# Performance work log

Measured on AMD Instinct MI355X. Metric: run time of the kernel, lower is better.

Reference implementation:

```python
import jax, jax.numpy as jnp
import numpy as np

NEG_SLOPE = 0.2  # PyG GATConv default negative_slope


def gat_conv(x, edge_index, W, att_src, att_dst, bias):
    # PyG GATConv, heads=1, add_self_loops=True, lin bias=False, final bias added
    N = x.shape[0]
    h = x @ W                                     # [N, F]
    loops = jnp.arange(N, dtype=edge_index.dtype)
    src = jnp.concatenate([edge_index[0], loops])
    dst = jnp.concatenate([edge_index[1], loops])
    a_src = h @ att_src                           # [N]
    a_dst = h @ att_dst                           # [N]
    e = a_src[src] + a_dst[dst]
    e = jnp.where(e > 0, e, NEG_SLOPE * e)        # leaky_relu
    m = jax.ops.segment_max(e, dst, num_segments=N)
    w = jnp.exp(e - m[dst])
    denom = jax.ops.segment_sum(w, dst, num_segments=N)
    alpha = w / denom[dst]
    out = jax.ops.segment_sum(h[src] * alpha[:, None], dst, num_segments=N)
    return out + bias


def gcn_conv(x, edge_index, W, b):
    # PyG GCNConv: add self-loops + symmetric normalization
    N = x.shape[0]
    loops = jnp.arange(N, dtype=edge_index.dtype)
    src = jnp.concatenate([edge_index[0], loops])
    dst = jnp.concatenate([edge_index[1], loops])
    deg = jax.ops.segment_sum(jnp.ones(src.shape[0], dtype=x.dtype), dst, num_segments=N)
    dinv = jax.lax.rsqrt(jnp.maximum(deg, 1e-12))  # deg >= 1 thanks to self-loops
    norm = dinv[src] * dinv[dst]
    xw = x @ W
    return jax.ops.segment_sum(xw[src] * norm[:, None], dst, num_segments=N) + b


def get_final_node(x, batch, num_graphs):
    nn_ = jax.ops.segment_sum(jnp.ones(x.shape[0], dtype=jnp.int32), batch, num_segments=num_graphs)
    cum = jnp.concatenate([jnp.zeros(1, dtype=nn_.dtype), jnp.cumsum(nn_)[:-1]])
    return x[cum]


def ontology_emb(table, e1, e2, W, asrc, adst, b, idx_map):
    emb = gat_conv(table, e1, W, asrc, adst, b)
    emb = gat_conv(emb, e2, W, asrc, adst, b)
    return emb[idx_map]


def _forward(spec_emb, diag_table, proce_table, atc_table,
             diag_W, diag_asrc, diag_adst, diag_b,
             proce_W, proce_asrc, proce_adst, proce_b,
             atc_W, atc_asrc, atc_adst, atc_b,
             gcn_W1, gcn_b1, gcn_W2, gcn_b2, gcn_W3, gcn_b3,
             diag_e1, diag_e2, proce_e1, proce_e2, atc_e1, atc_e2,
             diag_map, proce_map, atc_map,
             left_x, left_graph_index, right_x, right_graph_index,
             left_x_batch, right_x_batch, num_graphs):
    diag_emb = ontology_emb(diag_table, diag_e1, diag_e2, diag_W, diag_asrc, diag_adst, diag_b, diag_map)
    proce_emb = ontology_emb(proce_table, proce_e1, proce_e2, proce_W, proce_asrc, proce_adst, proce_b, proce_map)
    atc_emb = ontology_emb(atc_table, atc_e1, atc_e2, atc_W, atc_asrc, atc_adst, atc_b, atc_map)
    all_emb = jnp.concatenate([spec_emb, diag_emb, proce_emb, atc_emb], axis=0)
    lh = all_emb[left_x[:, 0]]   # squeeze(dim=1)
    rh = all_emb[right_x[:, 0]]
    for W, b in ((gcn_W1, gcn_b1), (gcn_W2, gcn_b2), (gcn_W3, gcn_b3)):
        lh = gcn_conv(lh, left_graph_index, W, b)
        rh = gcn_conv(rh, right_graph_index, W, b)
    lf = get_final_node(lh, left_x_batch, num_graphs)
    rf = get_final_node(rh, right_x_batch, num_graphs)
    eps = 1e-6  # CosineSimilarity eps
    num = jnp.sum(lf * rf, axis=-1)
    den = jnp.maximum(jnp.linalg.norm(lf, axis=-1), eps) * jnp.maximum(jnp.linalg.norm(rf, axis=-1), eps)
    return num / den


def setup_inputs() -> dict:
    key = jax.random.key(0)
    ks = jax.random.split(key, 32)
    HID = 128
    B, NPG = 2048, 50
    N = B * NPG               # 102400 nodes per side
    E_PAT = 409600            # 4 edges per node
    DIAG_N, DIAG_L = 30000, 20000
    PROCE_N, PROCE_L = 12000, 8000
    ATC_N, ATC_L = 6000, 4000
    ALL = 1 + DIAG_L + PROCE_L + ATC_L
    f = lambda k, s: jax.random.normal(k, s, dtype=jnp.float32)
    scale = 0.1
    inp = {
        'spec_emb': f(ks[0], (1, HID)),
        'diag_table': f(ks[1], (DIAG_N, HID)),
        'proce_table': f(ks[2], (PROCE_N, HID)),
        'atc_table': f(ks[3], (ATC_N, HID)),
    }
    for i, nm in enumerate(['diag', 'proce', 'atc']):
        inp[nm + '_W'] = f(ks[4 + i], (HID, HID)) * scale
        inp[nm + '_asrc'] = f(ks[7 + i], (HID,)) * scale
        inp[nm + '_adst'] = f(ks[10 + i], (HID,)) * scale
        inp[nm + '_b'] = jnp.zeros((HID,), jnp.float32)
    for j in range(3):
        inp['gcn_W%d' % (j + 1)] = f(ks[13 + j], (HID, HID)) * scale
        inp['gcn_b%d' % (j + 1)] = jnp.zeros((HID,), jnp.float32)
    inp['diag_e1'] = jax.random.randint(ks[16], (2, DIAG_N), 0, DIAG_N, dtype=jnp.int32)
    inp['diag_e2'] = jax.random.randint(ks[17], (2, DIAG_N), 0, DIAG_N, dtype=jnp.int32)
    inp['proce_e1'] = jax.random.randint(ks[18], (2, PROCE_N), 0, PROCE_N, dtype=jnp.int32)
    inp['proce_e2'] = jax.random.randint(ks[19], (2, PROCE_N), 0, PROCE_N, dtype=jnp.int32)
    inp['atc_e1'] = jax.random.randint(ks[20], (2, ATC_N), 0, ATC_N, dtype=jnp.int32)
    inp['atc_e2'] = jax.random.randint(ks[21], (2, ATC_N), 0, ATC_N, dtype=jnp.int32)
    inp['diag_map'] = jnp.arange(DIAG_L, dtype=jnp.int32)
    inp['proce_map'] = jnp.arange(PROCE_L, dtype=jnp.int32)
    inp['atc_map'] = jnp.arange(ATC_L, dtype=jnp.int32)
    inp['left_x'] = jax.random.randint(ks[22], (N, 1), 0, ALL, dtype=jnp.int32)
    inp['right_x'] = jax.random.randint(ks[23], (N, 1), 0, ALL, dtype=jnp.int32)
    inp['left_graph_index'] = jax.random.randint(ks[24], (2, E_PAT), 0, N, dtype=jnp.int32)
    inp['right_graph_index'] = jax.random.randint(ks[25], (2, E_PAT), 0, N, dtype=jnp.int32)
    batch = jnp.repeat(jnp.arange(B, dtype=jnp.int32), NPG)
    inp['left_x_batch'] = batch
    inp['right_x_batch'] = batch
    inp['num_graphs'] = B
    return inp


def reference(spec_emb, diag_table, proce_table, atc_table,
              diag_W, diag_asrc, diag_adst, diag_b,
              proce_W, proce_asrc, proce_adst, proce_b,
              atc_W, atc_asrc, atc_adst, atc_b,
              gcn_W1, gcn_b1, gcn_W2, gcn_b2, gcn_W3, gcn_b3,
              diag_e1, diag_e2, proce_e1, proce_e2, atc_e1, atc_e2,
              diag_map, proce_map, atc_map,
              left_x, left_graph_index, right_x, right_graph_index,
              left_x_batch, right_x_batch, num_graphs):
    return _forward(spec_emb, diag_table, proce_table, atc_table,
                    diag_W, diag_asrc, diag_adst, diag_b,
                    proce_W, proce_asrc, proce_adst, proce_b,
                    atc_W, atc_asrc, atc_adst, atc_b,
                    gcn_W1, gcn_b1, gcn_W2, gcn_b2, gcn_W3, gcn_b3,
                    diag_e1, diag_e2, proce_e1, proce_e2, atc_e1, atc_e2,
                    diag_map, proce_map, atc_map,
                    left_x, left_graph_index, right_x, right_graph_index,
                    left_x_batch, right_x_batch, num_graphs)
```

## Files before the change

kernel.cpp:

```cpp
#include <hip/hip_runtime.h>
#include <hip/hip_bf16.h>

#define HID 128

typedef unsigned int uint;
typedef unsigned short ushort;
typedef short short8 __attribute__((ext_vector_type(8)));
typedef float f32x4 __attribute__((ext_vector_type(4)));

static inline int cdiv_i(long a, long b) { return (int)((a + b - 1) / b); }
static inline int imax_i(int a, int b) { return a > b ? a : b; }

__device__ __forceinline__ float bf2f(uint hi) {
    return __builtin_bit_cast(float, hi << 16);
}
__device__ __forceinline__ ushort f2bf(float f) {
    uint u = __builtin_bit_cast(uint, f);
    u = (u + 0x7fffu + ((u >> 16) & 1u)) >> 16;
    return (ushort)u;
}

struct CsrDesc {
    const int* esrc[8];
    const int* edst[8];
    int ebase[9];
    int nbase[9];
    int totE;
};

template <typename AT>
__device__ __forceinline__ void load_afrag(const AT* __restrict__ A, long row,
                                           int koff, short8& af) {
    if constexpr (__is_same(AT, ushort)) {
        const uint4 raw = *(const uint4*)(A + row * 128 + koff);
        af = __builtin_bit_cast(short8, raw);
    } else {
        const float4* p = (const float4*)(A + row * 128 + koff);
        const float4 x0 = p[0], x1 = p[1];
        af[0] = (short)f2bf(x0.x); af[1] = (short)f2bf(x0.y);
        af[2] = (short)f2bf(x0.z); af[3] = (short)f2bf(x0.w);
        af[4] = (short)f2bf(x1.x); af[5] = (short)f2bf(x1.y);
        af[6] = (short)f2bf(x1.z); af[7] = (short)f2bf(x1.w);
    }
}

struct GOnto {
    const ushort* Wt0; const ushort* Wt1; const ushort* Wt2;
    const float* s0; const float* s1; const float* s2;
    const float* d0; const float* d1; const float* d2;
    int bs1, bs2;
    int r1, r2, r3;
};
// ... 57 lines not shown
                if (row < Mg) Hg[row * 128 + col] = f2bf(acc[mi][ni][reg]);
            }
        }
    }

    float asv[8], adv[8];
#pragma unroll
    for (int ni = 0; ni < 8; ++ni) {
        asv[ni] = avs[ni * 16 + r];
        adv[ni] = avd[ni * 16 + r];
    }
#pragma unroll
    for (int mi = 0; mi < 2; ++mi) {
#pragma unroll
        for (int reg = 0; reg < 4; ++reg) {
            float ps = 0.f, pd = 0.f;
#pragma unroll
            for (int ni = 0; ni < 8; ++ni) {
                ps += acc[mi][ni][reg] * asv[ni];
                pd += acc[mi][ni][reg] * adv[ni];
            }
#pragma unroll
            for (int o = 1; o < 16; o <<= 1) {
                ps += __shfl_xor(ps, o);
                pd += __shfl_xor(pd, o);
            }
            const long row = m0 + mi * 16 + q * 4 + reg;
            if (r == 0 && row < Mg) {
                as_o[rb + row] = ps;
                ad_o[rb + row] = pd;
            }
        }
    }
}

__global__ __launch_bounds__(256) void gemm_onto_l2(const ushort* __restrict__ x0,
                                                    const ushort* __restrict__ x1,
                                                    const ushort* __restrict__ x2,
                                                    GOnto g, ushort* __restrict__ H,
                                                    float* __restrict__ as_o,
                                                    float* __restrict__ ad_o) {
    gemm_onto_dev<ushort>(blockIdx.x, x0, x1, x2, g, H, as_o, ad_o);
}

struct EmbSrc {
    const float* spec; const ushort* oE;
    const int* m0; const int* m1; const int* m2;
    int lb2, lb3, r1, r2;
};

__device__ __forceinline__ short8 load_emb(const EmbSrc& e, long row, int koff) {
    short8 af;
    if (row == 0) {
        const float4* pp = (const float4*)(e.spec + koff);
        const float4 x0 = pp[0], x1 = pp[1];
        af[0] = (short)f2bf(x0.x); af[1] = (short)f2bf(x0.y);
        af[2] = (short)f2bf(x0.z); af[3] = (short)f2bf(x0.w);
        af[4] = (short)f2bf(x1.x); af[5] = (short)f2bf(x1.y);
        af[6] = (short)f2bf(x1.z); af[7] = (short)f2bf(x1.w);
        return af;
    }
    const int r = (int)row;
    const int seg = (r >= e.lb2) + (r >= e.lb3);
    const int local = r - ((seg == 0) ? 1 : (seg == 1) ? e.lb2 : e.lb3);
    const int* mp = (seg == 0) ? e.m0 : (seg == 1) ? e.m1 : e.m2;
    const int rb = (seg == 0) ? 0 : (seg == 1) ? e.r1 : e.r2;
    const long sr = (long)rb + mp[local];
    return __builtin_bit_cast(short8, *(const uint4*)(e.oE + sr * 128 + koff));
}

__device__ void gemm_pat_tile(const EmbSrc& es, const ushort* __restrict__ Wt,
                              ushort* __restrict__ C, long m0blk, long rowEnd) {
    const int tid = threadIdx.x;
    const int wave = tid >> 6, lane = tid & 63;
    const int r = lane & 15, q = lane >> 4;
// ... 47 lines not shown
    gemm_pat_tile(es, Wt, C, m0, M);
    if (m0 + 128 < M) gemm_pat_tile(es, Wt, C, m0 + 128, M);
}

__device__ __forceinline__ void fold1_dev(int idx, const float* __restrict__ W2,
                                          const float* __restrict__ b2,
                                          const float* __restrict__ W3,
                                          float* __restrict__ W23b) {
    if (idx >= 129 * 128) return;
    const int i = idx >> 7, j = idx & 127;
    const float* a = (i < 128) ? (W2 + i * 128) : b2;
    float s = 0.f;
#pragma unroll 8
    for (int k = 0; k < 128; ++k) s += a[k] * W3[k * 128 + j];
    W23b[idx] = s;
}

__device__ __forceinline__ void fold2_dev(int idx, const float* __restrict__ W1,
                                          const float* __restrict__ b1,
                                          const float* __restrict__ W23b,
                                          ushort* __restrict__ WpT,
                                          float* __restrict__ cbuf) {
    if (idx >= 130 * 128) return;
    const int i = idx >> 7, j = idx & 127;
    if (i == 129) { cbuf[128 + j] = W23b[128 * 128 + j]; return; }
    const float* a = (i < 128) ? (W1 + i * 128) : b1;
    float s = 0.f;
#pragma unroll 8
    for (int k = 0; k < 128; ++k) s += a[k] * W23b[k * 128 + j];
    if (i < 128) WpT[j * 128 + i] = f2bf(s);
    else cbuf[j] = s;
}

__device__ __forceinline__ void mark_dev(int i, const int* __restrict__ lEg,
                                         const int* __restrict__ rEg, int EP,
                                         int NP, int* __restrict__ mk,
                                         int testBit, int setBit) {
    int src, dst;
    if (i < 2 * EP) {
        const int side = i >= EP;
        const int e = i - side * EP;
        const int* eg = side ? rEg : lEg;
        src = side * NP + eg[e];
        dst = side * NP + eg[EP + e];
    } else if (i < 2 * EP + 2 * NP) {
        src = dst = i - 2 * EP;
    } else return;
    if (mk[dst] & testBit) {
        const int old = mk[src];
        if (!(old & setBit)) mk[src] = old | setBit;
    }
}

__device__ __forceinline__ void csr_count_dev(int i, const CsrDesc& d,
                                              int* __restrict__ cnt) {
    if (i >= d.totE) return;
    int li = 0;
#pragma unroll
    for (int k = 1; k < 8; ++k) li += (i >= d.ebase[k]);
    const int v = d.nbase[li] + d.edst[li][i - d.ebase[li]];
    atomicAdd(&cnt[v], 1);
}

struct PackPrep {
    const float* W2; const float* b2; const float* W3; float* W23b;
    const float* wsrc[3]; ushort* wt_out;
    int* cnt; int NV;
    const int* bL; const int* bR; int NP;
    int* gfL; int* gfR; int* mk;
    int nbF1, nbWT, nbInit;
};

__global__ __launch_bounds__(256) void k_prep(PackPrep p) {
    const int b = blockIdx.x, tid = threadIdx.x;
    if (b < p.nbF1) {
        fold1_dev(b * 256 + tid, p.W2, p.b2, p.W3, p.W23b);
    } else if (b < p.nbF1 + p.nbWT) {
        const int idx = (b - p.nbF1) * 256 + tid;
        if (idx < 3 * 16384) {
            const int m = idx >> 14;
            const int e = idx & 16383;
            const int n = e >> 7, k = e & 127;
            p.wt_out[idx] = f2bf(p.wsrc[m][k * 128 + n]);
        }
    } else {
        const int i = (b - p.nbF1 - p.nbWT) * 256 + tid;
        if (i < p.NV) p.cnt[i] = 0;
        if (i < 2 * p.NP) {
            const int side = i >= p.NP;
            const int ii = i - (side ? p.NP : 0);
            const int* bb = side ? p.bR : p.bL;
            int* gf = side ? p.gfR : p.gfL;
            const int cur = bb[ii];
            const int prev = (ii == 0) ? -1 : bb[ii - 1];
            int m = 0;
            if (cur > prev) {
                for (int g = prev + 1; g <= cur; ++g) gf[g] = ii;
                m = 1;
            }
            p.mk[i] = m;
        }
    }
}

struct PackBig {
    const float* x0; const float* x1; const float* x2;
    GOnto go; ushort* H; float* as_o; float* ad_o;
    const float* W1; const float* b1; const float* W23b;
    ushort* WpT; float* cbuf;
    CsrDesc dsc; int* cnt;
    const int* lEg; const int* rEg; int EP; int NP; int* mk;
    int nbGemm, nbF2, nbCnt;
};

__global__ __launch_bounds__(256) void k_big1(PackBig p) {
    const int b = blockIdx.x, tid = threadIdx.x;
    if (b < p.nbGemm) {
        gemm_onto_dev<float>(b, p.x0, p.x1, p.x2, p.go, p.H, p.as_o, p.ad_o);
    } else if (b < p.nbGemm + p.nbF2) {
        fold2_dev((b - p.nbGemm) * 256 + tid, p.W1, p.b1, p.W23b, p.WpT, p.cbuf);
    } else if (b < p.nbGemm + p.nbF2 + p.nbCnt) {
        csr_count_dev((b - p.nbGemm - p.nbF2) * 256 + tid, p.dsc, p.cnt);
    } else {
        mark_dev((b - p.nbGemm - p.nbF2 - p.nbCnt) * 256 + tid, p.lEg, p.rEg,
                 p.EP, p.NP, p.mk, 1, 2);
    }
}

__device__ void scan_tile_dev(const int* __restrict__ in, int* __restrict__ out,
                              int* __restrict__ bsum, int n, int pn0, int pcnt,
                              float* __restrict__ dinv, int tb, int tid,
                              int* sbuf) {
    const int base = tb * 1024 + tid * 4;
    int v[4];
    int s = 0;
#pragma unroll
    for (int k = 0; k < 4; ++k) {
        const int i = base + k;
        v[k] = (i < n) ? (in[i] + 1) : 0;
        if (i >= pn0 && i < pn0 + pcnt)
            dinv[i - pn0] = rsqrtf(fmaxf((float)v[k], 1e-12f));
        s += v[k];
    }
    sbuf[tid] = s;
    __syncthreads();
    int x = s;
    for (int o = 1; o < 256; o <<= 1) {
        const int t = (tid >= o) ? sbuf[tid - o] : 0;
        __syncthreads();
        x += t;
        sbuf[tid] = x;
        __syncthreads();
    }
    int run = x - s;
#pragma unroll
    for (int k = 0; k < 4; ++k) {
        const int i = base + k;
        if (i < n) out[i] = run;
        run += v[k];
    }
    if (tid == 255) bsum[tb] = x;
}

struct PackScan {
    const int* cnt; int* offs; int* bsum;
    int NV; int pn0; int pcnt; float* dinv;
    const int* lEg; const int* rEg; int EP; int NP; int* mk;
    int nbScan;
};

__global__ __launch_bounds__(256) void k_scan(PackScan p) {
    __shared__ int sbuf[256];
    const int b = blockIdx.x, tid = threadIdx.x;
    if (b < p.nbScan) {
        scan_tile_dev(p.cnt, p.offs, p.bsum, p.NV, p.pn0, p.pcnt, p.dinv, b,
                      tid, sbuf);
    } else {
        mark_dev((b - p.nbScan) * 256 + tid, p.lEg, p.rEg, p.EP, p.NP, p.mk,
                 2, 4);
    }
}

__global__ __launch_bounds__(256) void k_scanfin(int* __restrict__ out,
                                                 int* __restrict__ out2,
                                                 const int* __restrict__ bsum,
                                                 int n, int nbData) {
    __shared__ int sbuf[256];
    const int tb = blockIdx.x, tid = threadIdx.x;
    int pLim = tb < nbData ? tb : nbData;
    int pth = 0;
    for (int j = tid; j < pLim; j += 256) pth += bsum[j];
    sbuf[tid] = pth;
    __syncthreads();
    for (int o = 128; o > 0; o >>= 1) {
        if (tid < o) sbuf[tid] += sbuf[tid + o];
        __syncthreads();
    }
    const int prefix = sbuf[0];
    const int base = tb * 1024 + tid * 4;
#pragma unroll
    for (int k = 0; k < 4; ++k) {
        const int i = base + k;
        if (i < n) {
            const int v = out[i] + prefix;
            out[i] = v;
            out2[i] = v;
        } else if (i == n) {
            out[i] = prefix + ((tb < nbData) ? bsum[tb] : 0);
        }
    }
}

struct FillP {
    CsrDesc dsc;
    const int* offs; int* offs2; const int* cnt;
    int* srcl; int4* pedge; const float* dinv;
    const int* lx; const int* rx; const int* mk;
    int NP, pB;
    int eStart, eCount, vStart, vCount;
};

__device__ void fill_dev(const FillP& f, int idx) {
    if (idx < f.eCount) {
        const int i = f.eStart + idx;
        int li = 0;
#pragma unroll
        for (int k = 1; k < 8; ++k) li += (i >= f.dsc.ebase[k]);
        const int j = i - f.dsc.ebase[li];
        const int v = f.dsc.nbase[li] + f.dsc.edst[li][j];
        const int s = f.dsc.esrc[li][j];
        if (li >= 6) {
            const int n2l = v - f.dsc.nbase[6];
            if (f.mk[n2l] == 0) return;
            const int sg = (li - 6) * f.NP + s;
            const int cidx = atomicAdd(&f.offs2[v], 1);
            int4 rec;
            rec.x = sg;
            rec.y = (li == 7 ? f.rx : f.lx)[s];
            rec.z = __float_as_int(f.dinv[n2l] * f.dinv[sg]);
            rec.w = 0;
            f.pedge[cidx - f.pB] = rec;
        } else {
            const int cidx = atomicAdd(&f.offs2[v], 1);
            f.srcl[cidx] = s;
        }
    } else if (idx < f.eCount + f.vCount) {
        const int v = f.vStart + (idx - f.eCount);
        int li = 0;
#pragma unroll
        for (int k = 1; k < 8; ++k) li += (v >= f.dsc.nbase[k]);
        const int s = v - f.dsc.nbase[li];
        if (li >= 6) {
            const int n2l = v - f.dsc.nbase[6];
            if (f.mk[n2l] == 0) return;
            const int cidx = f.offs[v] + f.cnt[v];
            const int sg = (li - 6) * f.NP + s;
            int4 rec;
            rec.x = sg;
            rec.y = (li == 7 ? f.rx : f.lx)[s];
            rec.z = __float_as_int(f.dinv[n2l] * f.dinv[sg]);
            rec.w = 0;
            f.pedge[cidx - f.pB] = rec;
        } else {
            f.srcl[f.offs[v] + f.cnt[v]] = s;
        }
    }
}

__global__ __launch_bounds__(256) void k_fill(FillP f) {
    fill_dev(f, blockIdx.x * 256 + threadIdx.x);
}

struct GatP {
    int r1, r2;
    int ob0, ob1, ob2;
    const float* b0; const float* b1; const float* b2;
};

__device__ __forceinline__ void acc8(float* acc, float w, const uint4 v) {
    acc[0] += w * bf2f(v.x & 0xffff);
    acc[1] += w * bf2f(v.x >> 16);
    acc[2] += w * bf2f(v.y & 0xffff);
    acc[3] += w * bf2f(v.y >> 16);
    acc[4] += w * bf2f(v.z & 0xffff);
    acc[5] += w * bf2f(v.z >> 16);
    acc[6] += w * bf2f(v.w & 0xffff);
    acc[7] += w * bf2f(v.w >> 16);
}

__device__ void gat_dev(int node, int ql, const ushort* __restrict__ h,
                        const float* __restrict__ as, const float* __restrict__ ad,
                        const int* __restrict__ offs, const int* __restrict__ srcl,
                        const GatP& p, ushort* __restrict__ out, int Mtot) {
    if (node >= Mtot) return;
    const int gid = (node >= p.r1) + (node >= p.r2);
    const int rb = (gid == 0) ? 0 : (gid == 1) ? p.r1 : p.r2;
    const int ob = (gid == 0) ? p.ob0 : (gid == 1) ? p.ob1 : p.ob2;
    const float* bias = (gid == 0) ? p.b0 : (gid == 1) ? p.b1 : p.b2;
    const int local = node - rb;
    const int beg = offs[ob + local], end = offs[ob + local + 1];
    const float adv = ad[node];
    float denom = 0.f;
    float acc[8] = {0.f, 0.f, 0.f, 0.f, 0.f, 0.f, 0.f, 0.f};
    int j = beg;
    for (; j + 2 <= end; j += 2) {
        const int s0 = srcl[j], s1 = srcl[j + 1];
        float e0 = as[rb + s0] + adv; e0 = (e0 > 0.f) ? e0 : 0.2f * e0;
        float e1 = as[rb + s1] + adv; e1 = (e1 > 0.f) ? e1 : 0.2f * e1;
        const float w0 = __expf(e0), w1 = __expf(e1);
        const uint4 v0 = *(const uint4*)(h + (size_t)(rb + s0) * 128 + ql * 8);
        const uint4 v1 = *(const uint4*)(h + (size_t)(rb + s1) * 128 + ql * 8);
        denom += w0 + w1;
        acc8(acc, w0, v0);
        acc8(acc, w1, v1);
    }
    if (j < end) {
        const int s0 = srcl[j];
        float e0 = as[rb + s0] + adv; e0 = (e0 > 0.f) ? e0 : 0.2f * e0;
        const float w0 = __expf(e0);
        const uint4 v0 = *(const uint4*)(h + (size_t)(rb + s0) * 128 + ql * 8);
        denom += w0;
        acc8(acc, w0, v0);
    }
    const float inv = 1.f / denom;
    const float4 bv0 = *(const float4*)(bias + ql * 8);
    const float4 bv1 = *(const float4*)(bias + ql * 8 + 4);
    uint4 o;
    o.x = (uint)f2bf(acc[0] * inv + bv0.x) | ((uint)f2bf(acc[1] * inv + bv0.y) << 16);
    o.y = (uint)f2bf(acc[2] * inv + bv0.z) | ((uint)f2bf(acc[3] * inv + bv0.w) << 16);
    o.z = (uint)f2bf(acc[4] * inv + bv1.x) | ((uint)f2bf(acc[5] * inv + bv1.y) << 16);
    o.w = (uint)f2bf(acc[6] * inv + bv1.z) | ((uint)f2bf(acc[7] * inv + bv1.w) << 16);
    *(uint4*)(out + (size_t)node * 128 + ql * 8) = o;
}

__global__ __launch_bounds__(256) void gat_all(const ushort* __restrict__ h,
                                               const float* __restrict__ as,
                                               const float* __restrict__ ad,
                                               const int* __restrict__ offs,
                                               const int* __restrict__ srcl,
                                               GatP p, ushort* __restrict__ out,
                                               int Mtot) {
    gat_dev(blockIdx.x * 16 + (threadIdx.x >> 4), threadIdx.x & 15, h, as, ad,
            offs, srcl, p, out, Mtot);
}

struct GatFill {
    const ushort* h; const float* as; const float* ad;
    const int* offs; const int* srcl;
    GatP gp; ushort* out; int Mtot; int nbGat;
    FillP f;
};

__global__ __launch_bounds__(256) void k_gat_fill(GatFill g) {
    const int b = blockIdx.x, tid = threadIdx.x;
    if (b < g.nbGat) {
        gat_dev(b * 16 + (tid >> 4), tid & 15, g.h, g.as, g.ad, g.offs, g.srcl,
                g.gp, g.out, g.Mtot);
    } else {
        fill_dev(g.f, (b - g.nbGat) * 256 + tid);
    }
}

__global__ __launch_bounds__(256) void gcn_agg1(const ushort* __restrict__ A3,
                                                const int4* __restrict__ pedge,
                                                const int* __restrict__ offs6,
                                                const float* __restrict__ c1,
                                                ushort* __restrict__ t1,
                                                const int* __restrict__ mk,
                                                int NP2, int pB) {
    const int n2 = blockIdx.x * 16 + (threadIdx.x >> 4);
    const int ql = threadIdx.x & 15;
    if (n2 >= NP2) return;
    if ((mk[n2] & 4) == 0) return;
    const int beg = offs6[n2] - pB, end = offs6[n2 + 1] - pB;
    float acc[8] = {0.f, 0.f, 0.f, 0.f, 0.f, 0.f, 0.f, 0.f};
    int j = beg;
    for (; j + 2 <= end; j += 2) {
        const int4 r0 = pedge[j], r1 = pedge[j + 1];
        const float w0 = __int_as_float(r0.z), w1 = __int_as_float(r1.z);
        const uint4 v0 = *(const uint4*)(A3 + (size_t)r0.y * 128 + ql * 8);
        const uint4 v1 = *(const uint4*)(A3 + (size_t)r1.y * 128 + ql * 8);
        acc8(acc, w0, v0);
        acc8(acc, w1, v1);
    }
    if (j < end) {
        const int4 r0 = pedge[j];
        const uint4 v0 = *(const uint4*)(A3 + (size_t)r0.y * 128 + ql * 8);
        acc8(acc, __int_as_float(r0.z), v0);
    }
    const float4 bv0 = *(const float4*)(c1 + ql * 8);
    const float4 bv1 = *(const float4*)(c1 + ql * 8 + 4);
    uint4 o;
    o.x = (uint)f2bf(acc[0] + bv0.x) | ((uint)f2bf(acc[1] + bv0.y) << 16);
    o.y = (uint)f2bf(acc[2] + bv0.z) | ((uint)f2bf(acc[3] + bv0.w) << 16);
    o.z = (uint)f2bf(acc[4] + bv1.x) | ((uint)f2bf(acc[5] + bv1.y) << 16);
    o.w = (uint)f2bf(acc[6] + bv1.z) | ((uint)f2bf(acc[7] + bv1.w) << 16);
    *(uint4*)(t1 + (size_t)n2 * 128 + ql * 8) = o;
}

__device__ __forceinline__ void gcn_q_acc(const ushort* __restrict__ x,
                                          const int4* __restrict__ pedge,
                                          int beg, int end, int ql, float* acc) {
    int j = beg;
    for (; j + 2 <= end; j += 2) {
        const int4 r0 = pedge[j], r1 = pedge[j + 1];
        const float w0 = __int_as_float(r0.z), w1 = __int_as_float(r1.z);
        const uint4 v0 = *(const uint4*)(x + (size_t)r0.x * 128 + ql * 8);
        const uint4 v1 = *(const uint4*)(x + (size_t)r1.x * 128 + ql * 8);
        acc8(acc, w0, v0);
        acc8(acc, w1, v1);
    }
    if (j < end) {
        const int4 r0 = pedge[j];
        const uint4 v0 = *(const uint4*)(x + (size_t)r0.x * 128 + ql * 8);
        acc8(acc, __int_as_float(r0.z), v0);
    }
}

__global__ __launch_bounds__(256) void gcn_agg2(const ushort* __restrict__ t1,
                                                const int4* __restrict__ pedge,
                                                const int* __restrict__ offs6,
                                                const float* __restrict__ c2,
                                                ushort* __restrict__ t2,
                                                const int* __restrict__ mk,
                                                int NP2, int pB) {
    const int n2 = blockIdx.x * 16 + (threadIdx.x >> 4);
    const int ql = threadIdx.x & 15;
    if (n2 >= NP2) return;
    if ((mk[n2] & 2) == 0) return;
    const int beg = offs6[n2] - pB, end = offs6[n2 + 1] - pB;
    float acc[8] = {0.f, 0.f, 0.f, 0.f, 0.f, 0.f, 0.f, 0.f};
    gcn_q_acc(t1, pedge, beg, end, ql, acc);
    const float4 bv0 = *(const float4*)(c2 + ql * 8);
    const float4 bv1 = *(const float4*)(c2 + ql * 8 + 4);
    uint4 o;
    o.x = (uint)f2bf(acc[0] + bv0.x) | ((uint)f2bf(acc[1] + bv0.y) << 16);
    o.y = (uint)f2bf(acc[2] + bv0.z) | ((uint)f2bf(acc[3] + bv0.w) << 16);
    o.z = (uint)f2bf(acc[4] + bv1.x) | ((uint)f2bf(acc[5] + bv1.y) << 16);
    o.w = (uint)f2bf(acc[6] + bv1.z) | ((uint)f2bf(acc[7] + bv1.w) << 16);
    *(uint4*)(t2 + (size_t)n2 * 128 + ql * 8) = o;
}

__global__ __launch_bounds__(256) void final_cos(const ushort* __restrict__ t2,
                                                 const int4* __restrict__ pedge,
                                                 const int* __restrict__ offs6,
                                                 const int* __restrict__ gfL,
                                                 const int* __restrict__ gfR,
                                                 const float* __restrict__ b3,
                                                 float* __restrict__ out,
                                                 int B, int NP, int pB) {
    const int g = blockIdx.x * 8 + (threadIdx.x >> 5);
    const int l32 = threadIdx.x & 31;
    const int side = l32 >> 4;
    const int ql = l32 & 15;
    if (g >= B) return;
    const int n2 = (side ? NP : 0) + (side ? gfR : gfL)[g];
    const int beg = offs6[n2] - pB, end = offs6[n2 + 1] - pB;
    float acc[8] = {0.f, 0.f, 0.f, 0.f, 0.f, 0.f, 0.f, 0.f};
    gcn_q_acc(t2, pedge, beg, end, ql, acc);
    const float4 bv0 = *(const float4*)(b3 + ql * 8);
    const float4 bv1 = *(const float4*)(b3 + ql * 8 + 4);
    float v[8];
    v[0] = acc[0] + bv0.x; v[1] = acc[1] + bv0.y;
    v[2] = acc[2] + bv0.z; v[3] = acc[3] + bv0.w;
    v[4] = acc[4] + bv1.x; v[5] = acc[5] + bv1.y;
    v[6] = acc[6] + bv1.z; v[7] = acc[7] + bv1.w;
    float num = 0.f, nself = 0.f, nother = 0.f;
#pragma unroll
    for (int j = 0; j < 8; ++j) {
        const float o = __shfl_xor(v[j], 16);
        num += v[j] * o;
        nself += v[j] * v[j];
        nother += o * o;
    }
#pragma unroll
    for (int o1 = 1; o1 < 16; o1 <<= 1) {
        num += __shfl_xor(num, o1);
        nself += __shfl_xor(nself, o1);
        nother += __shfl_xor(nother, o1);
    }
    if (l32 == 0)
        out[g] = num / (fmaxf(sqrtf(nself), 1e-6f) * fmaxf(sqrtf(nother), 1e-6f));
}

extern "C" void kernel_launch(void* const* d_in, const int* in_sizes, int n_in,
                              void* d_out, int out_size, void* d_ws, size_t ws_size,
                              hipStream_t stream) {
    (void)n_in; (void)ws_size;
    const float* spec = (const float*)d_in[0];
    const float* tabs[3] = {(const float*)d_in[1], (const float*)d_in[2], (const float*)d_in[3]};
    const float* ontW[3] = {(const float*)d_in[4], (const float*)d_in[8], (const float*)d_in[12]};
    const float* ontAs[3] = {(const float*)d_in[5], (const float*)d_in[9], (const float*)d_in[13]};
// ... 15 lines not shown
    int E1s[3] = {in_sizes[22] / 2, in_sizes[24] / 2, in_sizes[26] / 2};
    int E2s[3] = {in_sizes[23] / 2, in_sizes[25] / 2, in_sizes[27] / 2};
    int Ls[3] = {in_sizes[28], in_sizes[29], in_sizes[30]};
    const int NP = in_sizes[31];
    const int EP = in_sizes[33] / 2;
    const int B = out_size;
    const long ALL = 1 + (long)Ls[0] + Ls[1] + Ls[2];
    const int Mtot = Ms[0] + Ms[1] + Ms[2];
    const int r1 = Ms[0], r2 = Ms[0] + Ms[1];

    CsrDesc dsc;
    int eCnt[8], nCnt[8];
    for (int i = 0; i < 3; ++i) {
        dsc.esrc[i] = e1s[i];     dsc.edst[i] = e1s[i] + E1s[i];
        eCnt[i] = E1s[i];         nCnt[i] = Ms[i];
        dsc.esrc[3 + i] = e2s[i]; dsc.edst[3 + i] = e2s[i] + E2s[i];
        eCnt[3 + i] = E2s[i];     nCnt[3 + i] = Ms[i];
    }
    dsc.esrc[6] = left_eg;  dsc.edst[6] = left_eg + EP;  eCnt[6] = EP; nCnt[6] = NP;
    dsc.esrc[7] = right_eg; dsc.edst[7] = right_eg + EP; eCnt[7] = EP; nCnt[7] = NP;
    dsc.ebase[0] = 0;
    int nb_acc = 0;
    for (int i = 0; i < 8; ++i) {
        dsc.ebase[i + 1] = dsc.ebase[i] + eCnt[i];
        dsc.nbase[i] = nb_acc;
        nb_acc += nCnt[i];
    }
    const int NV = nb_acc;
    dsc.nbase[8] = NV;
    dsc.totE = dsc.ebase[8];
    const int totEntries = dsc.totE + NV;
    const int pB = dsc.ebase[6] + dsc.nbase[6];
    const int pEntries = totEntries - pB;

    char* ws = (char*)d_ws;
    size_t off = 0;
    auto alloc = [&](size_t bytes) -> void* {
        off = (off + 255) & ~(size_t)255;
        void* p = ws + off;
        off += bytes;
        return p;
    };
    ushort* wt4 = (ushort*)alloc((size_t)4 * 16384 * 2);
    float* W23b = (float*)alloc((size_t)129 * 128 * 4);
    float* cbuf = (float*)alloc((size_t)256 * 4);
    ushort* A3 = (ushort*)alloc((size_t)ALL * HID * 2);
    int* cnt = (int*)alloc((size_t)NV * 4);
    int* offs = (int*)alloc((size_t)(NV + 1) * 4);
    int* offs2 = (int*)alloc((size_t)NV * 4);
    int* srcl = (int*)alloc((size_t)pB * 4);
    int4* pedge = (int4*)alloc((size_t)pEntries * 16);
    int* bsum = (int*)alloc(1025 * 4);
    float* dinv = (float*)alloc((size_t)2 * NP * 4);
    float* as = (float*)alloc((size_t)Mtot * 4);
    float* ad = (float*)alloc((size_t)Mtot * 4);
    int* gfL = (int*)alloc((size_t)(B + 1) * 4);
    int* gfR = (int*)alloc((size_t)(B + 1) * 4);
    int* mk = (int*)alloc((size_t)2 * NP * 4);
    ushort* t1 = (ushort*)alloc((size_t)2 * NP * HID * 2);
    ushort* big = (ushort*)alloc((size_t)2 * NP * HID * 2);
    ushort* hbuf = big;
    ushort* obuf = big + (size_t)Mtot * HID;
    ushort* t2 = big;

    const ushort* wtOnt[3] = {wt4, wt4 + 16384, wt4 + 2 * 16384};
    ushort* WpT = wt4 + 3 * 16384;
    const float* c1 = cbuf;
    const float* c2 = cbuf + 128;

    PackPrep pp;
    pp.W2 = gcnW[1]; pp.b2 = gcnB[1]; pp.W3 = gcnW[2]; pp.W23b = W23b;
    pp.wsrc[0] = ontW[0]; pp.wsrc[1] = ontW[1]; pp.wsrc[2] = ontW[2];
    pp.wt_out = wt4;
    pp.cnt = cnt; pp.NV = NV;
    pp.bL = left_batch; pp.bR = right_batch; pp.NP = NP;
    pp.gfL = gfL; pp.gfR = gfR; pp.mk = mk;
    pp.nbF1 = cdiv_i(129 * 128, 256);
    pp.nbWT = cdiv_i(3 * 16384, 256);
    pp.nbInit = cdiv_i(imax_i(NV, 2 * NP), 256);
    k_prep<<<pp.nbF1 + pp.nbWT + pp.nbInit, 256, 0, stream>>>(pp);

    GOnto go;
    go.Wt0 = wtOnt[0]; go.Wt1 = wtOnt[1]; go.Wt2 = wtOnt[2];
    go.s0 = ontAs[0]; go.s1 = ontAs[1]; go.s2 = ontAs[2];
    go.d0 = ontAd[0]; go.d1 = ontAd[1]; go.d2 = ontAd[2];
    go.bs1 = cdiv_i(Ms[0], 128);
    go.bs2 = go.bs1 + cdiv_i(Ms[1], 128);
    const int totBlk = go.bs2 + cdiv_i(Ms[2], 128);
    go.r1 = r1; go.r2 = r2; go.r3 = Mtot;

    PackBig pg;
    pg.x0 = tabs[0]; pg.x1 = tabs[1]; pg.x2 = tabs[2];
    pg.go = go; pg.H = hbuf; pg.as_o = as; pg.ad_o = ad;
    pg.W1 = gcnW[0]; pg.b1 = gcnB[0]; pg.W23b = W23b;
    pg.WpT = WpT; pg.cbuf = cbuf;
    pg.dsc = dsc; pg.cnt = cnt;
    pg.lEg = left_eg; pg.rEg = right_eg; pg.EP = EP; pg.NP = NP; pg.mk = mk;
    pg.nbGemm = totBlk;
    pg.nbF2 = cdiv_i(130 * 128, 256);
    pg.nbCnt = cdiv_i(dsc.totE, 256);
    const int nbMark = cdiv_i(2 * EP + 2 * NP, 256);
    k_big1<<<pg.nbGemm + pg.nbF2 + pg.nbCnt + nbMark, 256, 0, stream>>>(pg);

    PackScan psn;
    psn.cnt = cnt; psn.offs = offs; psn.bsum = bsum;
    psn.NV = NV; psn.pn0 = dsc.nbase[6]; psn.pcnt = 2 * NP; psn.dinv = dinv;
    psn.lEg = left_eg; psn.rEg = right_eg; psn.EP = EP; psn.NP = NP; psn.mk = mk;
    psn.nbScan = cdiv_i(NV, 1024);
    k_scan<<<psn.nbScan + nbMark, 256, 0, stream>>>(psn);

    k_scanfin<<<cdiv_i(NV + 1, 1024), 256, 0, stream>>>(offs, offs2, bsum, NV,
                                                        psn.nbScan);

    FillP fb;
    fb.dsc = dsc; fb.offs = offs; fb.offs2 = offs2; fb.cnt = cnt;
    fb.srcl = srcl; fb.pedge = pedge; fb.dinv = dinv;
    fb.lx = left_x; fb.rx = right_x; fb.mk = mk;
    fb.NP = NP; fb.pB = pB;

    FillP fo = fb;
    fo.eStart = 0;             fo.eCount = dsc.ebase[3];
    fo.vStart = 0;             fo.vCount = dsc.nbase[3];
    k_fill<<<cdiv_i(fo.eCount + fo.vCount, 256), 256, 0, stream>>>(fo);

    GatFill gf;
    gf.h = hbuf; gf.as = as; gf.ad = ad; gf.offs = offs; gf.srcl = srcl;
    gf.gp = GatP{r1, r2, dsc.nbase[0], dsc.nbase[1], dsc.nbase[2],
                 ontB[0], ontB[1], ontB[2]};
    gf.out = obuf; gf.Mtot = Mtot;
    gf.nbGat = cdiv_i(Mtot, 16);
    gf.f = fb;
    gf.f.eStart = dsc.ebase[3]; gf.f.eCount = dsc.totE - dsc.ebase[3];
    gf.f.vStart = dsc.nbase[3]; gf.f.vCount = NV - dsc.nbase[3];
    k_gat_fill<<<gf.nbGat + cdiv_i(gf.f.eCount + gf.f.vCount, 256), 256, 0,
                 stream>>>(gf);

    gemm_onto_l2<<<totBlk, 256, 0, stream>>>(obuf, obuf + (size_t)r1 * HID,
                                             obuf + (size_t)r2 * HID, go, hbuf,
                                             as, ad);
    const GatP gp1{r1, r2, dsc.nbase[3], dsc.nbase[4], dsc.nbase[5],
                   ontB[0], ontB[1], ontB[2]};
    gat_all<<<cdiv_i(Mtot, 16), 256, 0, stream>>>(hbuf, as, ad, offs, srcl, gp1,
                                                  obuf, Mtot);

    EmbSrc es;
    es.spec = spec; es.oE = obuf;
    es.m0 = maps[0]; es.m1 = maps[1]; es.m2 = maps[2];
    es.lb2 = 1 + Ls[0]; es.lb3 = 1 + Ls[0] + Ls[1];
    es.r1 = r1; es.r2 = r2;
    gemm_pat<<<cdiv_i(ALL, 256), 256, 0, stream>>>(es, WpT, A3, (int)ALL);

    const int* offs6 = offs + dsc.nbase[6];
    gcn_agg1<<<cdiv_i(2 * NP, 16), 256, 0, stream>>>(A3, pedge, offs6, c1, t1,
                                                     mk, 2 * NP, pB);
    gcn_agg2<<<cdiv_i(2 * NP, 16), 256, 0, stream>>>(t1, pedge, offs6, c2, t2,
                                                     mk, 2 * NP, pB);
    final_cos<<<cdiv_i(B, 8), 256, 0, stream>>>(t2, pedge, offs6, gfL, gfR,
                                                gcnB[2], (float*)d_out, B, NP, pB);
}
```

Measured before the change: 334.3 us.

## Pack CSR counts into bytes and move GCN node marking onto built CSR

Per-node in-degree counters are packed four per 32-bit word, with byte-shifted atomics, and the scan reads them as one word per thread. The reachability marking that selects which GCN nodes need aggregating no longer runs as edge-list sweeps inside the count and scan kernels. It now walks the finished patient CSR backward from each graph's first node, and those passes are fused into the second-layer ontology GEMM and GAT kernels. The fill step now writes every patient edge record instead of only marked ones, which adds some write work. The byte counters silently overflow if any node has 255 or more incoming edges.

```diff
diff --git a/kernel.cpp b/kernel.cpp
--- a/kernel.cpp
+++ b/kernel.cpp
@@ -18,6 +18,10 @@
     uint u = __builtin_bit_cast(uint, f);
     u = (u + 0x7fffu + ((u >> 16) & 1u)) >> 16;
     return (ushort)u;
+}
+
+__device__ __forceinline__ int cnt_rd(const uint* __restrict__ cnt, int v) {
+    return (int)((cnt[v >> 2] >> ((v & 3) * 8)) & 0xffu);
 }
 
 struct CsrDesc {
@@ -141,15 +145,6 @@
             }
         }
     }
-}
-
-__global__ __launch_bounds__(256) void gemm_onto_l2(const ushort* __restrict__ x0,
-                                                    const ushort* __restrict__ x1,
-                                                    const ushort* __restrict__ x2,
-                                                    GOnto g, ushort* __restrict__ H,
-                                                    float* __restrict__ as_o,
-                                                    float* __restrict__ ad_o) {
-    gemm_onto_dev<ushort>(blockIdx.x, x0, x1, x2, g, H, as_o, ad_o);
 }
 
 struct EmbSrc {
@@ -263,40 +258,20 @@
     else cbuf[j] = s;
 }
 
-__device__ __forceinline__ void mark_dev(int i, const int* __restrict__ lEg,
-                                         const int* __restrict__ rEg, int EP,
-                                         int NP, int* __restrict__ mk,
-                                         int testBit, int setBit) {
-    int src, dst;
-    if (i < 2 * EP) {
-        const int side = i >= EP;
-        const int e = i - side * EP;
-        const int* eg = side ? rEg : lEg;
-        src = side * NP + eg[e];
-        dst = side * NP + eg[EP + e];
-    } else if (i < 2 * EP + 2 * NP) {
-        src = dst = i - 2 * EP;
-    } else return;
-    if (mk[dst] & testBit) {
-        const int old = mk[src];
-        if (!(old & setBit)) mk[src] = old | setBit;
-    }
-}
-
 __device__ __forceinline__ void csr_count_dev(int i, const CsrDesc& d,
-                                              int* __restrict__ cnt) {
+                                              uint* __restrict__ cnt) {
     if (i >= d.totE) return;
     int li = 0;
 #pragma unroll
     for (int k = 1; k < 8; ++k) li += (i >= d.ebase[k]);
     const int v = d.nbase[li] + d.edst[li][i - d.ebase[li]];
-    atomicAdd(&cnt[v], 1);
+    atomicAdd(&cnt[v >> 2], 1u << ((v & 3) * 8));
 }
 
 struct PackPrep {
     const float* W2; const float* b2; const float* W3; float* W23b;
     const float* wsrc[3]; ushort* wt_out;
-    int* cnt; int NV;
+    uint* cnt; int cntW;
     const int* bL; const int* bR; int NP;
     int* gfL; int* gfR; int* mk;
     int nbF1, nbWT, nbInit;
@@ -316,7 +291,7 @@
         }
     } else {
         const int i = (b - p.nbF1 - p.nbWT) * 256 + tid;
-        if (i < p.NV) p.cnt[i] = 0;
+        if (i < p.cntW) p.cnt[i] = 0;
         if (i < 2 * p.NP) {
             const int side = i >= p.NP;
             const int ii = i - (side ? p.NP : 0);
@@ -324,12 +299,9 @@
             int* gf = side ? p.gfR : p.gfL;
             const int cur = bb[ii];
             const int prev = (ii == 0) ? -1 : bb[ii - 1];
-            int m = 0;
-            if (cur > prev) {
+            if (cur > prev)
                 for (int g = prev + 1; g <= cur; ++g) gf[g] = ii;
-                m = 1;
-            }
-            p.mk[i] = m;
+            p.mk[i] = 0;
         }
     }
 }
@@ -339,9 +311,8 @@
     GOnto go; ushort* H; float* as_o; float* ad_o;
     const float* W1; const float* b1; const float* W23b;
     ushort* WpT; float* cbuf;
-    CsrDesc dsc; int* cnt;
-    const int* lEg; const int* rEg; int EP; int NP; int* mk;
-    int nbGemm, nbF2, nbCnt;
+    CsrDesc dsc; uint* cnt;
+    int nbGemm, nbF2;
 };
 
 __global__ __launch_bounds__(256) void k_big1(PackBig p) {
@@ -350,25 +321,26 @@
         gemm_onto_dev<float>(b, p.x0, p.x1, p.x2, p.go, p.H, p.as_o, p.ad_o);
     } else if (b < p.nbGemm + p.nbF2) {
         fold2_dev((b - p.nbGemm) * 256 + tid, p.W1, p.b1, p.W23b, p.WpT, p.cbuf);
-    } else if (b < p.nbGemm + p.nbF2 + p.nbCnt) {
+    } else {
         csr_count_dev((b - p.nbGemm - p.nbF2) * 256 + tid, p.dsc, p.cnt);
-    } else {
-        mark_dev((b - p.nbGemm - p.nbF2 - p.nbCnt) * 256 + tid, p.lEg, p.rEg,
-                 p.EP, p.NP, p.mk, 1, 2);
-    }
-}
-
-__device__ void scan_tile_dev(const int* __restrict__ in, int* __restrict__ out,
-                              int* __restrict__ bsum, int n, int pn0, int pcnt,
-                              float* __restrict__ dinv, int tb, int tid,
-                              int* sbuf) {
+    }
+}
+
+__global__ __launch_bounds__(256) void k_scan(const uint* __restrict__ in,
+                                              int* __restrict__ out,
+                                              int* __restrict__ bsum, int n,
+                                              int pn0, int pcnt,
+                                              float* __restrict__ dinv) {
+    __shared__ int sbuf[256];
+    const int tb = blockIdx.x, tid = threadIdx.x;
     const int base = tb * 1024 + tid * 4;
+    const uint word = in[tb * 256 + tid];
     int v[4];
     int s = 0;
 #pragma unroll
     for (int k = 0; k < 4; ++k) {
         const int i = base + k;
-        v[k] = (i < n) ? (in[i] + 1) : 0;
+        v[k] = (i < n) ? (int)((word >> (k * 8)) & 0xffu) + 1 : 0;
         if (i >= pn0 && i < pn0 + pcnt)
             dinv[i - pn0] = rsqrtf(fmaxf((float)v[k], 1e-12f));
         s += v[k];
@@ -391,25 +363,6 @@
         run += v[k];
     }
     if (tid == 255) bsum[tb] = x;
-}
-
-struct PackScan {
-    const int* cnt; int* offs; int* bsum;
-    int NV; int pn0; int pcnt; float* dinv;
-    const int* lEg; const int* rEg; int EP; int NP; int* mk;
-    int nbScan;
-};
-
-__global__ __launch_bounds__(256) void k_scan(PackScan p) {
-    __shared__ int sbuf[256];
-    const int b = blockIdx.x, tid = threadIdx.x;
-    if (b < p.nbScan) {
-        scan_tile_dev(p.cnt, p.offs, p.bsum, p.NV, p.pn0, p.pcnt, p.dinv, b,
-                      tid, sbuf);
-    } else {
-        mark_dev((b - p.nbScan) * 256 + tid, p.lEg, p.rEg, p.EP, p.NP, p.mk,
-                 2, 4);
-    }
 }
 
 __global__ __launch_bounds__(256) void k_scanfin(int* __restrict__ out,
@@ -444,9 +397,9 @@
 
 struct FillP {
     CsrDesc dsc;
-    const int* offs; int* offs2; const int* cnt;
+    const int* offs; int* offs2; const uint* cnt;
     int* srcl; int4* pedge; const float* dinv;
-    const int* lx; const int* rx; const int* mk;
+    const int* lx; const int* rx;
     int NP, pB;
     int eStart, eCount, vStart, vCount;
 };
@@ -460,31 +413,9 @@
         const int j = i - f.dsc.ebase[li];
         const int v = f.dsc.nbase[li] + f.dsc.edst[li][j];
         const int s = f.dsc.esrc[li][j];
+        const int cidx = atomicAdd(&f.offs2[v], 1);
         if (li >= 6) {
             const int n2l = v - f.dsc.nbase[6];
-            if (f.mk[n2l] == 0) return;
-            const int sg = (li - 6) * f.NP + s;
-            const int cidx = atomicAdd(&f.offs2[v], 1);
-            int4 rec;
-            rec.x = sg;
-            rec.y = (li == 7 ? f.rx : f.lx)[s];
-            rec.z = __float_as_int(f.dinv[n2l] * f.dinv[sg]);
-            rec.w = 0;
-            f.pedge[cidx - f.pB] = rec;
-        } else {
-            const int cidx = atomicAdd(&f.offs2[v], 1);
-            f.srcl[cidx] = s;
-        }
-    } else if (idx < f.eCount + f.vCount) {
-        const int v = f.vStart + (idx - f.eCount);
-        int li = 0;
-#pragma unroll
-        for (int k = 1; k < 8; ++k) li += (v >= f.dsc.nbase[k]);
-        const int s = v - f.dsc.nbase[li];
-        if (li >= 6) {
-            const int n2l = v - f.dsc.nbase[6];
-            if (f.mk[n2l] == 0) return;
-            const int cidx = f.offs[v] + f.cnt[v];
             const int sg = (li - 6) * f.NP + s;
             int4 rec;
             rec.x = sg;
@@ -493,13 +424,62 @@
             rec.w = 0;
             f.pedge[cidx - f.pB] = rec;
         } else {
-            f.srcl[f.offs[v] + f.cnt[v]] = s;
+            f.srcl[cidx] = s;
+        }
+    } else if (idx < f.eCount + f.vCount) {
+        const int v = f.vStart + (idx - f.eCount);
+        int li = 0;
+#pragma unroll
+        for (int k = 1; k < 8; ++k) li += (v >= f.dsc.nbase[k]);
+        const int s = v - f.dsc.nbase[li];
+        const int cidx = f.offs[v] + cnt_rd(f.cnt, v);
+        if (li >= 6) {
+            const int n2l = v - f.dsc.nbase[6];
+            const int sg = (li - 6) * f.NP + s;
+            int4 rec;
+            rec.x = sg;
+            rec.y = (li == 7 ? f.rx : f.lx)[s];
+            rec.z = __float_as_int(f.dinv[n2l] * f.dinv[sg]);
+            rec.w = 0;
+            f.pedge[cidx - f.pB] = rec;
+        } else {
+            f.srcl[cidx] = s;
         }
     }
 }
 
 __global__ __launch_bounds__(256) void k_fill(FillP f) {
     fill_dev(f, blockIdx.x * 256 + threadIdx.x);
+}
+
+__device__ void markA_dev(int i, const int* __restrict__ gfL,
+                          const int* __restrict__ gfR, int B, int NP,
+                          const int* __restrict__ offs6,
+                          const int4* __restrict__ pedge, int pB,
+                          int* __restrict__ mk) {
+    if (i >= 2 * B) return;
+    const int side = i >= B;
+    const int g = i - side * B;
+    const int n2 = (side ? NP : 0) + (side ? gfR : gfL)[g];
+    const int beg = offs6[n2] - pB, end = offs6[n2 + 1] - pB;
+    for (int j = beg; j < end; ++j) {
+        const int s = pedge[j].x;
+        const int old = mk[s];
+        if (!(old & 2)) mk[s] = old | 2;
+    }
+}
+
+__device__ void markB_dev(int n2, const int* __restrict__ offs6,
+                          const int4* __restrict__ pedge, int pB,
+                          int* __restrict__ mk, int NP2) {
+    if (n2 >= NP2) return;
+    if (!(mk[n2] & 2)) return;
+    const int beg = offs6[n2] - pB, end = offs6[n2 + 1] - pB;
+    for (int j = beg; j < end; ++j) {
+        const int s = pedge[j].x;
+        const int old = mk[s];
+        if (!(old & 4)) mk[s] = old | 4;
+    }
 }
 
 struct GatP {
@@ -564,17 +544,6 @@
     *(uint4*)(out + (size_t)node * 128 + ql * 8) = o;
 }
 
-__global__ __launch_bounds__(256) void gat_all(const ushort* __restrict__ h,
-                                               const float* __restrict__ as,
-                                               const float* __restrict__ ad,
-                                               const int* __restrict__ offs,
-                                               const int* __restrict__ srcl,
-                                               GatP p, ushort* __restrict__ out,
-                                               int Mtot) {
-    gat_dev(blockIdx.x * 16 + (threadIdx.x >> 4), threadIdx.x & 15, h, as, ad,
-            offs, srcl, p, out, Mtot);
-}
-
 struct GatFill {
     const ushort* h; const float* as; const float* ad;
     const int* offs; const int* srcl;
@@ -589,6 +558,65 @@
                 g.gp, g.out, g.Mtot);
     } else {
         fill_dev(g.f, (b - g.nbGat) * 256 + tid);
+    }
+}
+
+struct GemmMarkA {
+    const ushort* x0; const ushort* x1; const ushort* x2;
+    GOnto go; ushort* H; float* as_o; float* ad_o;
+    const int* gfL; const int* gfR; int B; int NP;
+    const int* offs6; const int4* pedge; int pB; int* mk;
+    int nbGemm;
+};
+
+__global__ __launch_bounds__(256) void k_gemm2_markA(GemmMarkA p) {
+    const int b = blockIdx.x;
+    if (b < p.nbGemm) {
+        gemm_onto_dev<ushort>(b, p.x0, p.x1, p.x2, p.go, p.H, p.as_o, p.ad_o);
+    } else {
+        markA_dev((b - p.nbGemm) * 256 + threadIdx.x, p.gfL, p.gfR, p.B, p.NP,
+                  p.offs6, p.pedge, p.pB, p.mk);
+    }
+}
+
+struct GatMarkB {
+    const ushort* h; const float* as; const float* ad;
+    const int* offs; const int* srcl;
+    GatP gp; ushort* out; int Mtot; int nbGat;
+    const int* offs6; const int4* pedge; int pB; int* mk; int NP2;
+};
+
+__global__ __launch_bounds__(256) void k_gat2_markB(GatMarkB p) {
+    const int b = blockIdx.x, tid = threadIdx.x;
+    if (b < p.nbGat) {
+        gat_dev(b * 16 + (tid >> 4), tid & 15, p.h, p.as, p.ad, p.offs, p.srcl,
+                p.gp, p.out, p.Mtot);
+    } else {
+        markB_dev((b - p.nbGat) * 256 + tid, p.offs6, p.pedge, p.pB, p.mk,
+                  p.NP2);
+    }
+}
+
+__device__ __forceinline__ void gcn_q_acc(const ushort* __restrict__ x,
+                                          const int4* __restrict__ pedge,
+                                          int beg, int end, int ql, float* acc,
+                                          bool useY) {
+    int j = beg;
+    for (; j + 2 <= end; j += 2) {
+        const int4 r0 = pedge[j], r1 = pedge[j + 1];
+        const float w0 = __int_as_float(r0.z), w1 = __int_as_float(r1.z);
+        const int i0 = useY ? r0.y : r0.x;
+        const int i1 = useY ? r1.y : r1.x;
+        const uint4 v0 = *(const uint4*)(x + (size_t)i0 * 128 + ql * 8);
+        const uint4 v1 = *(const uint4*)(x + (size_t)i1 * 128 + ql * 8);
+        acc8(acc, w0, v0);
+        acc8(acc, w1, v1);
+    }
+    if (j < end) {
+        const int4 r0 = pedge[j];
+        const int i0 = useY ? r0.y : r0.x;
+        const uint4 v0 = *(const uint4*)(x + (size_t)i0 * 128 + ql * 8);
+        acc8(acc, __int_as_float(r0.z), v0);
     }
 }
 
@@ -605,20 +633,7 @@
     if ((mk[n2] & 4) == 0) return;
     const int beg = offs6[n2] - pB, end = offs6[n2 + 1] - pB;
     float acc[8] = {0.f, 0.f, 0.f, 0.f, 0.f, 0.f, 0.f, 0.f};
-    int j = beg;
-    for (; j + 2 <= end; j += 2) {
-        const int4 r0 = pedge[j], r1 = pedge[j + 1];
-        const float w0 = __int_as_float(r0.z), w1 = __int_as_float(r1.z);
-        const uint4 v0 = *(const uint4*)(A3 + (size_t)r0.y * 128 + ql * 8);
-        const uint4 v1 = *(const uint4*)(A3 + (size_t)r1.y * 128 + ql * 8);
-        acc8(acc, w0, v0);
-        acc8(acc, w1, v1);
-    }
-    if (j < end) {
-        const int4 r0 = pedge[j];
-        const uint4 v0 = *(const uint4*)(A3 + (size_t)r0.y * 128 + ql * 8);
-        acc8(acc, __int_as_float(r0.z), v0);
-    }
+    gcn_q_acc(A3, pedge, beg, end, ql, acc, true);
     const float4 bv0 = *(const float4*)(c1 + ql * 8);
     const float4 bv1 = *(const float4*)(c1 + ql * 8 + 4);
     uint4 o;
@@ -627,25 +642,6 @@
     o.z = (uint)f2bf(acc[4] + bv1.x) | ((uint)f2bf(acc[5] + bv1.y) << 16);
     o.w = (uint)f2bf(acc[6] + bv1.z) | ((uint)f2bf(acc[7] + bv1.w) << 16);
     *(uint4*)(t1 + (size_t)n2 * 128 + ql * 8) = o;
-}
-
-__device__ __forceinline__ void gcn_q_acc(const ushort* __restrict__ x,
-                                          const int4* __restrict__ pedge,
-                                          int beg, int end, int ql, float* acc) {
-    int j = beg;
-    for (; j + 2 <= end; j += 2) {
-        const int4 r0 = pedge[j], r1 = pedge[j + 1];
-        const float w0 = __int_as_float(r0.z), w1 = __int_as_float(r1.z);
-        const uint4 v0 = *(const uint4*)(x + (size_t)r0.x * 128 + ql * 8);
-        const uint4 v1 = *(const uint4*)(x + (size_t)r1.x * 128 + ql * 8);
-        acc8(acc, w0, v0);
-        acc8(acc, w1, v1);
-    }
-    if (j < end) {
-        const int4 r0 = pedge[j];
-        const uint4 v0 = *(const uint4*)(x + (size_t)r0.x * 128 + ql * 8);
-        acc8(acc, __int_as_float(r0.z), v0);
-    }
 }
 
 __global__ __launch_bounds__(256) void gcn_agg2(const ushort* __restrict__ t1,
@@ -661,7 +657,7 @@
     if ((mk[n2] & 2) == 0) return;
     const int beg = offs6[n2] - pB, end = offs6[n2 + 1] - pB;
     float acc[8] = {0.f, 0.f, 0.f, 0.f, 0.f, 0.f, 0.f, 0.f};
-    gcn_q_acc(t1, pedge, beg, end, ql, acc);
+    gcn_q_acc(t1, pedge, beg, end, ql, acc, false);
     const float4 bv0 = *(const float4*)(c2 + ql * 8);
     const float4 bv1 = *(const float4*)(c2 + ql * 8 + 4);
     uint4 o;
@@ -688,7 +684,7 @@
     const int n2 = (side ? NP : 0) + (side ? gfR : gfL)[g];
     const int beg = offs6[n2] - pB, end = offs6[n2 + 1] - pB;
     float acc[8] = {0.f, 0.f, 0.f, 0.f, 0.f, 0.f, 0.f, 0.f};
-    gcn_q_acc(t2, pedge, beg, end, ql, acc);
+    gcn_q_acc(t2, pedge, beg, end, ql, acc, false);
     const float4 bv0 = *(const float4*)(b3 + ql * 8);
     const float4 bv1 = *(const float4*)(b3 + ql * 8 + 4);
     float v[8];
@@ -770,6 +766,8 @@
     const int totEntries = dsc.totE + NV;
     const int pB = dsc.ebase[6] + dsc.nbase[6];
     const int pEntries = totEntries - pB;
+    const int nbScan = cdiv_i(NV, 1024);
+    const int cntW = nbScan * 256;
 
     char* ws = (char*)d_ws;
     size_t off = 0;
@@ -783,7 +781,7 @@
     float* W23b = (float*)alloc((size_t)129 * 128 * 4);
     float* cbuf = (float*)alloc((size_t)256 * 4);
     ushort* A3 = (ushort*)alloc((size_t)ALL * HID * 2);
-    int* cnt = (int*)alloc((size_t)NV * 4);
+    uint* cnt = (uint*)alloc((size_t)cntW * 4);
     int* offs = (int*)alloc((size_t)(NV + 1) * 4);
     int* offs2 = (int*)alloc((size_t)NV * 4);
     int* srcl = (int*)alloc((size_t)pB * 4);
@@ -805,17 +803,18 @@
     ushort* WpT = wt4 + 3 * 16384;
     const float* c1 = cbuf;
     const float* c2 = cbuf + 128;
+    const int* offs6 = offs + dsc.nbase[6];
 
     PackPrep pp;
     pp.W2 = gcnW[1]; pp.b2 = gcnB[1]; pp.W3 = gcnW[2]; pp.W23b = W23b;
     pp.wsrc[0] = ontW[0]; pp.wsrc[1] = ontW[1]; pp.wsrc[2] = ontW[2];
     pp.wt_out = wt4;
-    pp.cnt = cnt; pp.NV = NV;
+    pp.cnt = cnt; pp.cntW = cntW;
     pp.bL = left_batch; pp.bR = right_batch; pp.NP = NP;
     pp.gfL = gfL; pp.gfR = gfR; pp.mk = mk;
     pp.nbF1 = cdiv_i(129 * 128, 256);
     pp.nbWT = cdiv_i(3 * 16384, 256);
-    pp.nbInit = cdiv_i(imax_i(NV, 2 * NP), 256);
+    pp.nbInit = cdiv_i(imax_i(cntW, 2 * NP), 256);
     k_prep<<<pp.nbF1 + pp.nbWT + pp.nbInit, 256, 0, stream>>>(pp);
 
     GOnto go;
@@ -833,27 +832,21 @@
     pg.W1 = gcnW[0]; pg.b1 = gcnB[0]; pg.W23b = W23b;
     pg.WpT = WpT; pg.cbuf = cbuf;
     pg.dsc = dsc; pg.cnt = cnt;
-    pg.lEg = left_eg; pg.rEg = right_eg; pg.EP = EP; pg.NP = NP; pg.mk = mk;
     pg.nbGemm = totBlk;
     pg.nbF2 = cdiv_i(130 * 128, 256);
-    pg.nbCnt = cdiv_i(dsc.totE, 256);
-    const int nbMark = cdiv_i(2 * EP + 2 * NP, 256);
-    k_big1<<<pg.nbGemm + pg.nbF2 + pg.nbCnt + nbMark, 256, 0, stream>>>(pg);
-
-    PackScan psn;
-    psn.cnt = cnt; psn.offs = offs; psn.bsum = bsum;
-    psn.NV = NV; psn.pn0 = dsc.nbase[6]; psn.pcnt = 2 * NP; psn.dinv = dinv;
-    psn.lEg = left_eg; psn.rEg = right_eg; psn.EP = EP; psn.NP = NP; psn.mk = mk;
-    psn.nbScan = cdiv_i(NV, 1024);
-    k_scan<<<psn.nbScan + nbMark, 256, 0, stream>>>(psn);
+    const int nbCnt = cdiv_i(dsc.totE, 256);
+    k_big1<<<pg.nbGemm + pg.nbF2 + nbCnt, 256, 0, stream>>>(pg);
+
+    k_scan<<<nbScan, 256, 0, stream>>>(cnt, offs, bsum, NV, dsc.nbase[6],
+                                       2 * NP, dinv);
 
     k_scanfin<<<cdiv_i(NV + 1, 1024), 256, 0, stream>>>(offs, offs2, bsum, NV,
-                                                        psn.nbScan);
+                                                        nbScan);
 
     FillP fb;
     fb.dsc = dsc; fb.offs = offs; fb.offs2 = offs2; fb.cnt = cnt;
     fb.srcl = srcl; fb.pedge = pedge; fb.dinv = dinv;
-    fb.lx = left_x; fb.rx = right_x; fb.mk = mk;
+    fb.lx = left_x; fb.rx = right_x;
     fb.NP = NP; fb.pB = pB;
 
     FillP fo = fb;
@@ -873,13 +866,23 @@
     k_gat_fill<<<gf.nbGat + cdiv_i(gf.f.eCount + gf.f.vCount, 256), 256, 0,
                  stream>>>(gf);
 
-    gemm_onto_l2<<<totBlk, 256, 0, stream>>>(obuf, obuf + (size_t)r1 * HID,
-                                             obuf + (size_t)r2 * HID, go, hbuf,
-                                             as, ad);
-    const GatP gp1{r1, r2, dsc.nbase[3], dsc.nbase[4], dsc.nbase[5],
-                   ontB[0], ontB[1], ontB[2]};
-    gat_all<<<cdiv_i(Mtot, 16), 256, 0, stream>>>(hbuf, as, ad, offs, srcl, gp1,
-                                                  obuf, Mtot);
+    GemmMarkA gm;
+    gm.x0 = obuf; gm.x1 = obuf + (size_t)r1 * HID; gm.x2 = obuf + (size_t)r2 * HID;
+    gm.go = go; gm.H = hbuf; gm.as_o = as; gm.ad_o = ad;
+    gm.gfL = gfL; gm.gfR = gfR; gm.B = B; gm.NP = NP;
+    gm.offs6 = offs6; gm.pedge = pedge; gm.pB = pB; gm.mk = mk;
+    gm.nbGemm = totBlk;
+    k_gemm2_markA<<<totBlk + cdiv_i(2 * B, 256), 256, 0, stream>>>(gm);
+
+    GatMarkB gb;
+    gb.h = hbuf; gb.as = as; gb.ad = ad; gb.offs = offs; gb.srcl = srcl;
+    gb.gp = GatP{r1, r2, dsc.nbase[3], dsc.nbase[4], dsc.nbase[5],
+                 ontB[0], ontB[1], ontB[2]};
+    gb.out = obuf; gb.Mtot = Mtot;
+    gb.nbGat = cdiv_i(Mtot, 16);
+    gb.offs6 = offs6; gb.pedge = pedge; gb.pB = pB; gb.mk = mk;
+    gb.NP2 = 2 * NP;
+    k_gat2_markB<<<gb.nbGat + cdiv_i(2 * NP, 256), 256, 0, stream>>>(gb);
 
     EmbSrc es;
     es.spec = spec; es.oE = obuf;
@@ -888,7 +891,6 @@
     es.r1 = r1; es.r2 = r2;
     gemm_pat<<<cdiv_i(ALL, 256), 256, 0, stream>>>(es, WpT, A3, (int)ALL);
 
-    const int* offs6 = offs + dsc.nbase[6];
     gcn_agg1<<<cdiv_i(2 * NP, 16), 256, 0, stream>>>(A3, pedge, offs6, c1, t1,
                                                      mk, 2 * NP, pB);
     gcn_agg2<<<cdiv_i(2 * NP, 16), 256, 0, stream>>>(t1, pedge, offs6, c2, t2,
```

Measured after the change: 353.9 us. 1.06x slower.
